# Kernel optimization log

Hardware: AMD Instinct MI355X
Metric: run time of the kernel (lower is better)

Reference implementation:

```python
import jax, jax.numpy as jnp
from jax import lax
import numpy as np

H = 64  # hidden_dim


def _lstm_dir(x, W_ih, W_hh, b, reverse):
    # x: [B,T,I]; W_ih: [4H,I]; W_hh: [4H,H]; b: [4H] (b_ih+b_hh combined)
    B = x.shape[0]
    xp = jnp.einsum('bti,gi->btg', x, W_ih) + b          # [B,T,4H]
    xp = jnp.swapaxes(xp, 0, 1)                          # [T,B,4H]

    def step(carry, xt):
        h, c = carry
        g = xt + h @ W_hh.T                              # [B,4H]
        i, f, gg, o = jnp.split(g, 4, axis=-1)           # PyTorch gate order i,f,g,o
        i = jax.nn.sigmoid(i)
        f = jax.nn.sigmoid(f)
        gg = jnp.tanh(gg)
        o = jax.nn.sigmoid(o)
        c = f * c + i * gg
        h = o * jnp.tanh(c)
        return (h, c), h

    init = (jnp.zeros((B, H), x.dtype), jnp.zeros((B, H), x.dtype))
    _, hs = lax.scan(step, init, xp, reverse=reverse)    # outputs aligned to original positions
    return jnp.swapaxes(hs, 0, 1)                        # [B,T,H]


def _bilstm_layer(x, Wih_f, Whh_f, b_f, Wih_b, Whh_b, b_b):
    fwd = _lstm_dir(x, Wih_f, Whh_f, b_f, reverse=False)
    bwd = _lstm_dir(x, Wih_b, Whh_b, b_b, reverse=True)
    return jnp.concatenate([fwd, bwd], axis=-1)          # [B,T,2H]


def setup_inputs() -> dict:
    key = jax.random.key(0)
    ks = jax.random.split(key, 16)
    s = 0.1
    d = {}
    d['x'] = jax.random.normal(ks[0], (512, 512, 4), dtype=jnp.float32)
    # layer 0 (input size 4), forward / backward directions
    d['Wih_l0_f'] = jax.random.normal(ks[1], (4 * H, 4)) * s
    d['Whh_l0_f'] = jax.random.normal(ks[2], (4 * H, H)) * s
    d['b_l0_f'] = jax.random.normal(ks[3], (4 * H,)) * s
    d['Wih_l0_b'] = jax.random.normal(ks[4], (4 * H, 4)) * s
    d['Whh_l0_b'] = jax.random.normal(ks[5], (4 * H, H)) * s
    d['b_l0_b'] = jax.random.normal(ks[6], (4 * H,)) * s
    # layer 1 (input size 2H = 128)
    d['Wih_l1_f'] = jax.random.normal(ks[7], (4 * H, 2 * H)) * s
    d['Whh_l1_f'] = jax.random.normal(ks[8], (4 * H, H)) * s
    d['b_l1_f'] = jax.random.normal(ks[9], (4 * H,)) * s
    d['Wih_l1_b'] = jax.random.normal(ks[10], (4 * H, 2 * H)) * s
    d['Whh_l1_b'] = jax.random.normal(ks[11], (4 * H, H)) * s
    d['b_l1_b'] = jax.random.normal(ks[12], (4 * H,)) * s
    # final linear: 2H -> 1
    d['fc_w'] = jax.random.normal(ks[13], (1, 2 * H)) * s
    d['fc_b'] = jax.random.normal(ks[14], (1,)) * s
    return d


def reference(x, Wih_l0_f, Whh_l0_f, b_l0_f, Wih_l0_b, Whh_l0_b, b_l0_b,
              Wih_l1_f, Whh_l1_f, b_l1_f, Wih_l1_b, Whh_l1_b, b_l1_b,
              fc_w, fc_b):
    h0 = _bilstm_layer(x, Wih_l0_f, Whh_l0_f, b_l0_f, Wih_l0_b, Whh_l0_b, b_l0_b)
    h1 = _bilstm_layer(h0, Wih_l1_f, Whh_l1_f, b_l1_f, Wih_l1_b, Whh_l1_b, b_l1_b)
    pooled = jnp.mean(h1, axis=1)                        # [B,2H]
    return pooled @ fc_w.T + fc_b                        # [B,1]
```

## Files before the change

kernel.cpp:

```cpp
#include <hip/hip_runtime.h>

#define H  64
#define TT 512
#define BB 512
#define CSTR 80
#define UCH 16
#define XSTRF 260
#define NCHUNK (TT / UCH)

typedef _Float16 half8 __attribute__((ext_vector_type(8)));
typedef float    f32x4 __attribute__((ext_vector_type(4)));

__device__ __forceinline__ float frcp(float x) { return __builtin_amdgcn_rcpf(x); }
__device__ __forceinline__ float sigm(float x) { return frcp(1.f + __expf(-x)); }
__device__ __forceinline__ float tanh_fast(float x) { return 1.f - 2.f * frcp(__expf(2.f * x) + 1.f); }

__device__ __forceinline__ void step_barrier() {
    asm volatile("s_waitcnt lgkmcnt(0)\n\ts_barrier" ::: "memory");
}

__global__ __launch_bounds__(256) void xpad_prep(const float* __restrict__ x,
                                                 _Float16* __restrict__ xpad) {
    int gid = blockIdx.x * 256 + threadIdx.x;
    int row = gid >> 2, q = gid & 3;
    half8 v = {0,0,0,0,0,0,0,0};
    if (q == 0) {
        float4 xv = ((const float4*)x)[row];
        v[0] = (_Float16)xv.x; v[1] = (_Float16)xv.y;
        v[2] = (_Float16)xv.z; v[3] = (_Float16)xv.w;
    }
    *(half8*)(xpad + (size_t)row * 32 + q * 8) = v;
}

__global__ __launch_bounds__(256, 1) void lstm_l0(
    const _Float16* __restrict__ xpad,
    const float* __restrict__ WihF, const float* __restrict__ WhhF, const float* __restrict__ bF,
    const float* __restrict__ WihB, const float* __restrict__ WhhB, const float* __restrict__ bB,
    _Float16* __restrict__ out0)
{
    const int dir = blockIdx.x & 1;
    const int b0  = (blockIdx.x >> 1) * 4;
    const int tid = threadIdx.x;
    const int w = tid >> 6, l = tid & 63, m = l & 15, q = l >> 4;
    const int ch  = m & 3;
    const int ubo = m >> 2;
    const int uo  = w * 16 + ubo * 4 + q;

    const float* Wih = dir ? WihB : WihF;
    const float* Whh = dir ? WhhB : WhhF;
    const float* bia = dir ? bB   : bF;

    half8 Ah[4][2];
#pragma unroll
    for (int ub = 0; ub < 4; ++ub) {
        const int wrow = (m & 3) * 64 + (w * 16 + ub * 4 + (m >> 2));
#pragma unroll
        for (int s2 = 0; s2 < 2; ++s2) {
            const float* src = Whh + wrow * 64 + s2 * 32 + q * 8;
            half8 tmp;
#pragma unroll
            for (int j = 0; j < 8; ++j) tmp[j] = (_Float16)src[j];
            Ah[ub][s2] = tmp;
        }
    }

    half8 Bg[4];
    float bvj[4];
#pragma unroll
    for (int j = 0; j < 4; ++j) {
        const int n  = w * 64 + j * 16 + m;
        const int gr = (n & 3) * 64 + (n >> 2);
        bvj[j] = bia[gr];
        half8 tmp;
#pragma unroll
        for (int jj = 0; jj < 8; ++jj) {
            int k = q * 8 + jj;
            tmp[jj] = (k < 4) ? (_Float16)Wih[gr * 4 + k] : (_Float16)0.f;
        }
        Bg[j] = tmp;
    }

    __shared__ __align__(16) float xp[4][UCH][XSTRF];
    __shared__ __align__(16) _Float16 hbuf[2][4][CSTR];
    for (int i = tid; i < 2 * 4 * CSTR / 2; i += 256) ((unsigned int*)hbuf)[i] = 0u;
    __syncthreads();

    float c = 0.f;
    int p = 0;

    half8 a[4];
    {
        const int tA = dir ? (TT - 1 - m) : m;
#pragma unroll
        for (int cc = 0; cc < 4; ++cc)
            a[cc] = *(const half8*)(xpad + (size_t)((b0 + cc) * TT + tA) * 32 + q * 8);
    }

    for (int chunk = 0; chunk < NCHUNK; ++chunk) {
        const int c0 = chunk * UCH;

#pragma unroll
        for (int cc = 0; cc < 4; ++cc) {
#pragma unroll
            for (int j = 0; j < 4; ++j) {
                f32x4 acc = {bvj[j], bvj[j], bvj[j], bvj[j]};
                acc = __builtin_amdgcn_mfma_f32_16x16x32_f16(a[cc], Bg[j], acc, 0, 0, 0);
#pragma unroll
                for (int i = 0; i < 4; ++i)
                    xp[cc][q * 4 + i][w * 64 + j * 16 + m] = acc[i];
            }
        }
        if (chunk + 1 < NCHUNK) {
            const int c0n = c0 + UCH;
            const int tA = dir ? (TT - 1 - (c0n + m)) : (c0n + m);
#pragma unroll
            for (int cc = 0; cc < 4; ++cc)
                a[cc] = *(const half8*)(xpad + (size_t)((b0 + cc) * TT + tA) * 32 + q * 8);
        }

        f32x4 xv = *(const f32x4*)&xp[ch][0][uo * 4];
        for (int u = 0; u < UCH; ++u) {
            int un = (u + 1 < UCH) ? (u + 1) : u;
            f32x4 xn = *(const f32x4*)&xp[ch][un][uo * 4];

            half8 ah0 = *(const half8*)&hbuf[p][ch][q * 8];
            half8 ah1 = *(const half8*)&hbuf[p][ch][32 + q * 8];

            f32x4 g_own;
#pragma unroll
            for (int ub = 0; ub < 4; ++ub) {
                f32x4 g = __builtin_amdgcn_mfma_f32_16x16x32_f16(Ah[ub][0], ah0, xv, 0, 0, 0);
                g       = __builtin_amdgcn_mfma_f32_16x16x32_f16(Ah[ub][1], ah1, g, 0, 0, 0);
                if (ub == ubo) g_own = g;
            }

            float e_i = sigm(g_own[0]), e_f = sigm(g_own[1]);
            float e_g = tanh_fast(g_own[2]), e_o = sigm(g_own[3]);
            c = e_f * c + e_i * e_g;
            float hh = e_o * tanh_fast(c);

            const int tg = dir ? (TT - 1 - (c0 + u)) : (c0 + u);
            out0[((size_t)(b0 + ch) * TT + tg) * 128 + dir * 64 + uo] = (_Float16)hh;
            hbuf[p ^ 1][ch][uo] = (_Float16)hh;
            step_barrier();
            p ^= 1; xv = xn;
        }
    }
}

__global__ __launch_bounds__(256, 1) void lstm_l1(
    const _Float16* __restrict__ out0,
    const float* __restrict__ WihF, const float* __restrict__ WhhF, const float* __restrict__ bF,
    const float* __restrict__ WihB, const float* __restrict__ WhhB, const float* __restrict__ bB,
    float* __restrict__ pooled)
{
    const int dir = blockIdx.x & 1;
    const int b0  = (blockIdx.x >> 1) * 4;
    const int tid = threadIdx.x;
    const int w = tid >> 6, l = tid & 63, m = l & 15, q = l >> 4;
    const int ch  = m & 3;
    const int ubo = m >> 2;
    const int uo  = w * 16 + ubo * 4 + q;

    const float* Wih = dir ? WihB : WihF;
    const float* Whh = dir ? WhhB : WhhF;
    const float* bia = dir ? bB   : bF;

    half8 Ah[4][2];
#pragma unroll
    for (int ub = 0; ub < 4; ++ub) {
        const int wrow = (m & 3) * 64 + (w * 16 + ub * 4 + (m >> 2));
#pragma unroll
        for (int s2 = 0; s2 < 2; ++s2) {
            const float* src = Whh + wrow * 64 + s2 * 32 + q * 8;
            half8 tmp;
#pragma unroll
            for (int j = 0; j < 8; ++j) tmp[j] = (_Float16)src[j];
            Ah[ub][s2] = tmp;
        }
    }

    half8 Bg[4][4];
    float bvj[4];
#pragma unroll
    for (int j = 0; j < 4; ++j) {
        const int n  = w * 64 + j * 16 + m;
        const int gr = (n & 3) * 64 + (n >> 2);
        bvj[j] = bia[gr];
#pragma unroll
        for (int k4 = 0; k4 < 4; ++k4) {
            const float* src = Wih + gr * 128 + k4 * 32 + q * 8;
            half8 tmp;
#pragma unroll
            for (int jj = 0; jj < 8; ++jj) tmp[jj] = (_Float16)src[jj];
            Bg[j][k4] = tmp;
        }
    }

    __shared__ __align__(16) float xp[4][UCH][XSTRF];
    __shared__ __align__(16) _Float16 hbuf[2][4][CSTR];
    for (int i = tid; i < 2 * 4 * CSTR / 2; i += 256) ((unsigned int*)hbuf)[i] = 0u;
    __syncthreads();

    float c = 0.f, hs = 0.f;
    int p = 0;

    half8 a[4][4];
    {
        const int tA = dir ? (TT - 1 - m) : m;
#pragma unroll
        for (int cc = 0; cc < 4; ++cc) {
            const _Float16* arow = out0 + (size_t)((b0 + cc) * TT + tA) * 128 + q * 8;
#pragma unroll
            for (int k4 = 0; k4 < 4; ++k4)
                a[cc][k4] = *(const half8*)(arow + k4 * 32);
        }
    }

    for (int chunk = 0; chunk < NCHUNK; ++chunk) {
        const int c0 = chunk * UCH;

#pragma unroll
        for (int cc = 0; cc < 4; ++cc) {
#pragma unroll
            for (int j = 0; j < 4; ++j) {
                f32x4 acc = {bvj[j], bvj[j], bvj[j], bvj[j]};
                acc = __builtin_amdgcn_mfma_f32_16x16x32_f16(a[cc][0], Bg[j][0], acc, 0, 0, 0);
                acc = __builtin_amdgcn_mfma_f32_16x16x32_f16(a[cc][1], Bg[j][1], acc, 0, 0, 0);
                acc = __builtin_amdgcn_mfma_f32_16x16x32_f16(a[cc][2], Bg[j][2], acc, 0, 0, 0);
                acc = __builtin_amdgcn_mfma_f32_16x16x32_f16(a[cc][3], Bg[j][3], acc, 0, 0, 0);
#pragma unroll
                for (int i = 0; i < 4; ++i)
                    xp[cc][q * 4 + i][w * 64 + j * 16 + m] = acc[i];
            }
        }
        if (chunk + 1 < NCHUNK) {
            const int c0n = c0 + UCH;
            const int tA = dir ? (TT - 1 - (c0n + m)) : (c0n + m);
#pragma unroll
            for (int cc = 0; cc < 4; ++cc) {
                const _Float16* arow = out0 + (size_t)((b0 + cc) * TT + tA) * 128 + q * 8;
#pragma unroll
                for (int k4 = 0; k4 < 4; ++k4)
                    a[cc][k4] = *(const half8*)(arow + k4 * 32);
            }
        }

        f32x4 xv = *(const f32x4*)&xp[ch][0][uo * 4];
        for (int u = 0; u < UCH; ++u) {
            int un = (u + 1 < UCH) ? (u + 1) : u;
            f32x4 xn = *(const f32x4*)&xp[ch][un][uo * 4];

            half8 ah0 = *(const half8*)&hbuf[p][ch][q * 8];
            half8 ah1 = *(const half8*)&hbuf[p][ch][32 + q * 8];

            f32x4 g_own;
#pragma unroll
            for (int ub = 0; ub < 4; ++ub) {
                f32x4 g = __builtin_amdgcn_mfma_f32_16x16x32_f16(Ah[ub][0], ah0, xv, 0, 0, 0);
                g       = __builtin_amdgcn_mfma_f32_16x16x32_f16(Ah[ub][1], ah1, g, 0, 0, 0);
                if (ub == ubo) g_own = g;
            }

            float e_i = sigm(g_own[0]), e_f = sigm(g_own[1]);
            float e_g = tanh_fast(g_own[2]), e_o = sigm(g_own[3]);
            c = e_f * c + e_i * e_g;
            float hh = e_o * tanh_fast(c);
            hs += hh;

            hbuf[p ^ 1][ch][uo] = (_Float16)hh;
            step_barrier();
            p ^= 1; xv = xn;
        }
    }

    pooled[(size_t)(b0 + ch) * 128 + dir * 64 + uo] = hs;
}

__global__ __launch_bounds__(64) void fc_head(
    const float* __restrict__ pooled,
    const float* __restrict__ fcw, const float* __restrict__ fcb,
    float* __restrict__ out)
{
    const int b = blockIdx.x;
    const int l = threadIdx.x;
    float v = pooled[b * 128 + l] * fcw[l] + pooled[b * 128 + 64 + l] * fcw[64 + l];
#pragma unroll
    for (int o = 32; o > 0; o >>= 1) v += __shfl_down(v, o);
    if (l == 0) out[b] = v * (1.f / (float)TT) + fcb[0];
}

extern "C" void kernel_launch(void* const* d_in, const int* in_sizes, int n_in,
                              void* d_out, int out_size, void* d_ws, size_t ws_size,
                              hipStream_t stream) {
    const float* x       = (const float*)d_in[0];
    const float* Wih_l0f = (const float*)d_in[1];
    const float* Whh_l0f = (const float*)d_in[2];
    const float* b_l0f   = (const float*)d_in[3];
    const float* Wih_l0b = (const float*)d_in[4];
    const float* Whh_l0b = (const float*)d_in[5];
    const float* b_l0b   = (const float*)d_in[6];
    const float* Wih_l1f = (const float*)d_in[7];
    const float* Whh_l1f = (const float*)d_in[8];
    const float* b_l1f   = (const float*)d_in[9];
    const float* Wih_l1b = (const float*)d_in[10];
    const float* Whh_l1b = (const float*)d_in[11];
    const float* b_l1b   = (const float*)d_in[12];
    const float* fcw     = (const float*)d_in[13];
    const float* fcb     = (const float*)d_in[14];

    const size_t o_xpad   = 0;
    const size_t o_out0   = o_xpad + (size_t)BB * TT * 32 * 2;
    const size_t o_pooled = o_out0 + (size_t)BB * TT * 128 * 2;

    _Float16* xpad   = (_Float16*)((char*)d_ws + o_xpad);
    _Float16* out0   = (_Float16*)((char*)d_ws + o_out0);
    float*    pooled = (float*)((char*)d_ws + o_pooled);

    xpad_prep<<<(BB * TT * 4) / 256, 256, 0, stream>>>(x, xpad);
    lstm_l0<<<(BB / 4) * 2, 256, 0, stream>>>(xpad, Wih_l0f, Whh_l0f, b_l0f,
                                              Wih_l0b, Whh_l0b, b_l0b, out0);
    lstm_l1<<<(BB / 4) * 2, 256, 0, stream>>>(out0, Wih_l1f, Whh_l1f, b_l1f,
                                              Wih_l1b, Whh_l1b, b_l1b, pooled);
    fc_head<<<BB, 64, 0, stream>>>(pooled, fcw, fcb, (float*)d_out);
}
```

Measured before the change: 450.8 us.

## Remap gate rows per MFMA tile, fold exp2 scales into weights, vectorize stores

Reorders the recurrent and input weight rows so each of the four MFMA output tiles holds one gate type. Each lane now updates four hidden units directly instead of selecting one tile's result and discarding the rest. The -log2e and 2·log2e factors are folded into the fp16 weights and biases, so the sigmoid and tanh use raw exp2 plus reciprocal, and the cell state is kept in a scaled domain. Hidden-state, output and pooled writes become half4/float4 vector stores from a quarter of the lanes. The trade-off is four times the transcendental work per lane per step on the serial critical path. A barrier is also added after the per-chunk xp writes.

```diff
diff --git a/kernel.cpp b/kernel.cpp
--- a/kernel.cpp
+++ b/kernel.cpp
@@ -5,15 +5,20 @@
 #define BB 512
 #define CSTR 80
 #define UCH 16
-#define XSTRF 260
+#define XROW 260
+#define XCH  (UCH*XROW + 8)
 #define NCHUNK (TT / UCH)
 
 typedef _Float16 half8 __attribute__((ext_vector_type(8)));
+typedef _Float16 half4 __attribute__((ext_vector_type(4)));
 typedef float    f32x4 __attribute__((ext_vector_type(4)));
 
+#define LOG2E 1.4426950408889634f
+#define TWOL  2.8853900817779268f
+#define FOURL 5.7707801635558536f
+
 __device__ __forceinline__ float frcp(float x) { return __builtin_amdgcn_rcpf(x); }
-__device__ __forceinline__ float sigm(float x) { return frcp(1.f + __expf(-x)); }
-__device__ __forceinline__ float tanh_fast(float x) { return 1.f - 2.f * frcp(__expf(2.f * x) + 1.f); }
+__device__ __forceinline__ float ex2(float x)  { return __builtin_amdgcn_exp2f(x); }
 
 __device__ __forceinline__ void step_barrier() {
     asm volatile("s_waitcnt lgkmcnt(0)\n\ts_barrier" ::: "memory");
@@ -42,9 +47,7 @@
     const int b0  = (blockIdx.x >> 1) * 4;
     const int tid = threadIdx.x;
     const int w = tid >> 6, l = tid & 63, m = l & 15, q = l >> 4;
-    const int ch  = m & 3;
-    const int ubo = m >> 2;
-    const int uo  = w * 16 + ubo * 4 + q;
+    const int ch = m & 3;
 
     const float* Wih = dir ? WihB : WihF;
     const float* Whh = dir ? WhhB : WhhF;
@@ -52,40 +55,41 @@
 
     half8 Ah[4][2];
 #pragma unroll
-    for (int ub = 0; ub < 4; ++ub) {
-        const int wrow = (m & 3) * 64 + (w * 16 + ub * 4 + (m >> 2));
+    for (int t = 0; t < 4; ++t) {
+        const float st = (t == 2) ? TWOL : -LOG2E;
+        const int wrow = t * 64 + w * 16 + m;
 #pragma unroll
         for (int s2 = 0; s2 < 2; ++s2) {
             const float* src = Whh + wrow * 64 + s2 * 32 + q * 8;
             half8 tmp;
 #pragma unroll
-            for (int j = 0; j < 8; ++j) tmp[j] = (_Float16)src[j];
-            Ah[ub][s2] = tmp;
-        }
-    }
-
+            for (int j = 0; j < 8; ++j) tmp[j] = (_Float16)(src[j] * st);
+            Ah[t][s2] = tmp;
+        }
+    }
+
+    const float sw = (w == 2) ? TWOL : -LOG2E;
     half8 Bg[4];
     float bvj[4];
 #pragma unroll
     for (int j = 0; j < 4; ++j) {
-        const int n  = w * 64 + j * 16 + m;
-        const int gr = (n & 3) * 64 + (n >> 2);
-        bvj[j] = bia[gr];
+        const int n = w * 64 + j * 16 + m;
+        bvj[j] = bia[n] * sw;
         half8 tmp;
 #pragma unroll
         for (int jj = 0; jj < 8; ++jj) {
             int k = q * 8 + jj;
-            tmp[jj] = (k < 4) ? (_Float16)Wih[gr * 4 + k] : (_Float16)0.f;
+            tmp[jj] = (k < 4) ? (_Float16)(Wih[n * 4 + k] * sw) : (_Float16)0.f;
         }
         Bg[j] = tmp;
     }
 
-    __shared__ __align__(16) float xp[4][UCH][XSTRF];
+    __shared__ __align__(16) float xp[4 * XCH];
     __shared__ __align__(16) _Float16 hbuf[2][4][CSTR];
     for (int i = tid; i < 2 * 4 * CSTR / 2; i += 256) ((unsigned int*)hbuf)[i] = 0u;
     __syncthreads();
 
-    float c = 0.f;
+    float cp[4] = {0.f, 0.f, 0.f, 0.f};
     int p = 0;
 
     half8 a[4];
@@ -107,43 +111,64 @@
                 acc = __builtin_amdgcn_mfma_f32_16x16x32_f16(a[cc], Bg[j], acc, 0, 0, 0);
 #pragma unroll
                 for (int i = 0; i < 4; ++i)
-                    xp[cc][q * 4 + i][w * 64 + j * 16 + m] = acc[i];
+                    xp[cc * XCH + (q * 4 + i) * XROW + w * 64 + j * 16 + m] = acc[i];
             }
         }
         if (chunk + 1 < NCHUNK) {
-            const int c0n = c0 + UCH;
-            const int tA = dir ? (TT - 1 - (c0n + m)) : (c0n + m);
+            const int tA = dir ? (TT - 1 - (c0 + UCH + m)) : (c0 + UCH + m);
 #pragma unroll
             for (int cc = 0; cc < 4; ++cc)
                 a[cc] = *(const half8*)(xpad + (size_t)((b0 + cc) * TT + tA) * 32 + q * 8);
         }
-
-        f32x4 xv = *(const f32x4*)&xp[ch][0][uo * 4];
+        step_barrier();
+
+        f32x4 xv[4];
+#pragma unroll
+        for (int t = 0; t < 4; ++t)
+            xv[t] = *(const f32x4*)&xp[ch * XCH + t * 64 + w * 16 + q * 4];
+
         for (int u = 0; u < UCH; ++u) {
-            int un = (u + 1 < UCH) ? (u + 1) : u;
-            f32x4 xn = *(const f32x4*)&xp[ch][un][uo * 4];
-
             half8 ah0 = *(const half8*)&hbuf[p][ch][q * 8];
             half8 ah1 = *(const half8*)&hbuf[p][ch][32 + q * 8];
 
-            f32x4 g_own;
-#pragma unroll
-            for (int ub = 0; ub < 4; ++ub) {
-                f32x4 g = __builtin_amdgcn_mfma_f32_16x16x32_f16(Ah[ub][0], ah0, xv, 0, 0, 0);
-                g       = __builtin_amdgcn_mfma_f32_16x16x32_f16(Ah[ub][1], ah1, g, 0, 0, 0);
-                if (ub == ubo) g_own = g;
-            }
-
-            float e_i = sigm(g_own[0]), e_f = sigm(g_own[1]);
-            float e_g = tanh_fast(g_own[2]), e_o = sigm(g_own[3]);
-            c = e_f * c + e_i * e_g;
-            float hh = e_o * tanh_fast(c);
-
-            const int tg = dir ? (TT - 1 - (c0 + u)) : (c0 + u);
-            out0[((size_t)(b0 + ch) * TT + tg) * 128 + dir * 64 + uo] = (_Float16)hh;
-            hbuf[p ^ 1][ch][uo] = (_Float16)hh;
+            const int un = (u + 1 < UCH) ? (u + 1) : u;
+            f32x4 xn[4];
+#pragma unroll
+            for (int t = 0; t < 4; ++t)
+                xn[t] = *(const f32x4*)&xp[ch * XCH + un * XROW + t * 64 + w * 16 + q * 4];
+
+            f32x4 g[4];
+#pragma unroll
+            for (int t = 0; t < 4; ++t) {
+                f32x4 acc = __builtin_amdgcn_mfma_f32_16x16x32_f16(Ah[t][0], ah0, xv[t], 0, 0, 0);
+                acc       = __builtin_amdgcn_mfma_f32_16x16x32_f16(Ah[t][1], ah1, acc,  0, 0, 0);
+                g[t] = acc;
+            }
+
+            float hh[4];
+#pragma unroll
+            for (int i = 0; i < 4; ++i) {
+                float e_i = frcp(1.f + ex2(g[0][i]));
+                float e_f = frcp(1.f + ex2(g[1][i]));
+                float tg  = TWOL - FOURL * frcp(1.f + ex2(g[2][i]));
+                float e_o = frcp(1.f + ex2(g[3][i]));
+                cp[i] = e_f * cp[i] + e_i * tg;
+                float r = frcp(1.f + ex2(cp[i]));
+                hh[i] = e_o * fmaf(-2.f, r, 1.f);
+            }
+
+            if (m < 4) {
+                half4 hv;
+                hv[0] = (_Float16)hh[0]; hv[1] = (_Float16)hh[1];
+                hv[2] = (_Float16)hh[2]; hv[3] = (_Float16)hh[3];
+                const int tg_t = dir ? (TT - 1 - (c0 + u)) : (c0 + u);
+                *(half4*)&out0[((size_t)(b0 + m) * TT + tg_t) * 128 + dir * 64 + w * 16 + q * 4] = hv;
+                *(half4*)&hbuf[p ^ 1][m][w * 16 + q * 4] = hv;
+            }
             step_barrier();
-            p ^= 1; xv = xn;
+            p ^= 1;
+#pragma unroll
+            for (int t = 0; t < 4; ++t) xv[t] = xn[t];
         }
     }
 }
@@ -158,9 +183,7 @@
     const int b0  = (blockIdx.x >> 1) * 4;
     const int tid = threadIdx.x;
     const int w = tid >> 6, l = tid & 63, m = l & 15, q = l >> 4;
-    const int ch  = m & 3;
-    const int ubo = m >> 2;
-    const int uo  = w * 16 + ubo * 4 + q;
+    const int ch = m & 3;
 
     const float* Wih = dir ? WihB : WihF;
     const float* Whh = dir ? WhhB : WhhF;
@@ -168,41 +191,43 @@
 
     half8 Ah[4][2];
 #pragma unroll
-    for (int ub = 0; ub < 4; ++ub) {
-        const int wrow = (m & 3) * 64 + (w * 16 + ub * 4 + (m >> 2));
+    for (int t = 0; t < 4; ++t) {
+        const float st = (t == 2) ? TWOL : -LOG2E;
+        const int wrow = t * 64 + w * 16 + m;
 #pragma unroll
         for (int s2 = 0; s2 < 2; ++s2) {
             const float* src = Whh + wrow * 64 + s2 * 32 + q * 8;
             half8 tmp;
 #pragma unroll
-            for (int j = 0; j < 8; ++j) tmp[j] = (_Float16)src[j];
-            Ah[ub][s2] = tmp;
-        }
-    }
-
+            for (int j = 0; j < 8; ++j) tmp[j] = (_Float16)(src[j] * st);
+            Ah[t][s2] = tmp;
+        }
+    }
+
+    const float sw = (w == 2) ? TWOL : -LOG2E;
     half8 Bg[4][4];
     float bvj[4];
 #pragma unroll
     for (int j = 0; j < 4; ++j) {
-        const int n  = w * 64 + j * 16 + m;
-        const int gr = (n & 3) * 64 + (n >> 2);
-        bvj[j] = bia[gr];
+        const int n = w * 64 + j * 16 + m;
+        bvj[j] = bia[n] * sw;
 #pragma unroll
         for (int k4 = 0; k4 < 4; ++k4) {
-            const float* src = Wih + gr * 128 + k4 * 32 + q * 8;
+            const float* src = Wih + n * 128 + k4 * 32 + q * 8;
             half8 tmp;
 #pragma unroll
-            for (int jj = 0; jj < 8; ++jj) tmp[jj] = (_Float16)src[jj];
+            for (int jj = 0; jj < 8; ++jj) tmp[jj] = (_Float16)(src[jj] * sw);
             Bg[j][k4] = tmp;
         }
     }
 
-    __shared__ __align__(16) float xp[4][UCH][XSTRF];
+    __shared__ __align__(16) float xp[4 * XCH];
     __shared__ __align__(16) _Float16 hbuf[2][4][CSTR];
     for (int i = tid; i < 2 * 4 * CSTR / 2; i += 256) ((unsigned int*)hbuf)[i] = 0u;
     __syncthreads();
 
-    float c = 0.f, hs = 0.f;
+    float cp[4] = {0.f, 0.f, 0.f, 0.f};
+    float hs[4] = {0.f, 0.f, 0.f, 0.f};
     int p = 0;
 
     half8 a[4][4];
@@ -231,12 +256,11 @@
                 acc = __builtin_amdgcn_mfma_f32_16x16x32_f16(a[cc][3], Bg[j][3], acc, 0, 0, 0);
 #pragma unroll
                 for (int i = 0; i < 4; ++i)
-                    xp[cc][q * 4 + i][w * 64 + j * 16 + m] = acc[i];
+                    xp[cc * XCH + (q * 4 + i) * XROW + w * 64 + j * 16 + m] = acc[i];
             }
         }
         if (chunk + 1 < NCHUNK) {
-            const int c0n = c0 + UCH;
-            const int tA = dir ? (TT - 1 - (c0n + m)) : (c0n + m);
+            const int tA = dir ? (TT - 1 - (c0 + UCH + m)) : (c0 + UCH + m);
 #pragma unroll
             for (int cc = 0; cc < 4; ++cc) {
                 const _Float16* arow = out0 + (size_t)((b0 + cc) * TT + tA) * 128 + q * 8;
@@ -245,36 +269,61 @@
                     a[cc][k4] = *(const half8*)(arow + k4 * 32);
             }
         }
-
-        f32x4 xv = *(const f32x4*)&xp[ch][0][uo * 4];
+        step_barrier();
+
+        f32x4 xv[4];
+#pragma unroll
+        for (int t = 0; t < 4; ++t)
+            xv[t] = *(const f32x4*)&xp[ch * XCH + t * 64 + w * 16 + q * 4];
+
         for (int u = 0; u < UCH; ++u) {
-            int un = (u + 1 < UCH) ? (u + 1) : u;
-            f32x4 xn = *(const f32x4*)&xp[ch][un][uo * 4];
-
             half8 ah0 = *(const half8*)&hbuf[p][ch][q * 8];
             half8 ah1 = *(const half8*)&hbuf[p][ch][32 + q * 8];
 
-            f32x4 g_own;
-#pragma unroll
-            for (int ub = 0; ub < 4; ++ub) {
-                f32x4 g = __builtin_amdgcn_mfma_f32_16x16x32_f16(Ah[ub][0], ah0, xv, 0, 0, 0);
-                g       = __builtin_amdgcn_mfma_f32_16x16x32_f16(Ah[ub][1], ah1, g, 0, 0, 0);
-                if (ub == ubo) g_own = g;
-            }
-
-            float e_i = sigm(g_own[0]), e_f = sigm(g_own[1]);
-            float e_g = tanh_fast(g_own[2]), e_o = sigm(g_own[3]);
-            c = e_f * c + e_i * e_g;
-            float hh = e_o * tanh_fast(c);
-            hs += hh;
-
-            hbuf[p ^ 1][ch][uo] = (_Float16)hh;
+            const int un = (u + 1 < UCH) ? (u + 1) : u;
+            f32x4 xn[4];
+#pragma unroll
+            for (int t = 0; t < 4; ++t)
+                xn[t] = *(const f32x4*)&xp[ch * XCH + un * XROW + t * 64 + w * 16 + q * 4];
+
+            f32x4 g[4];
+#pragma unroll
+            for (int t = 0; t < 4; ++t) {
+                f32x4 acc = __builtin_amdgcn_mfma_f32_16x16x32_f16(Ah[t][0], ah0, xv[t], 0, 0, 0);
+                acc       = __builtin_amdgcn_mfma_f32_16x16x32_f16(Ah[t][1], ah1, acc,  0, 0, 0);
+                g[t] = acc;
+            }
+
+            float hh[4];
+#pragma unroll
+            for (int i = 0; i < 4; ++i) {
+                float e_i = frcp(1.f + ex2(g[0][i]));
+                float e_f = frcp(1.f + ex2(g[1][i]));
+                float tg  = TWOL - FOURL * frcp(1.f + ex2(g[2][i]));
+                float e_o = frcp(1.f + ex2(g[3][i]));
+                cp[i] = e_f * cp[i] + e_i * tg;
+                float r = frcp(1.f + ex2(cp[i]));
+                hh[i] = e_o * fmaf(-2.f, r, 1.f);
+                hs[i] += hh[i];
+            }
+
+            if (m < 4) {
+                half4 hv;
+                hv[0] = (_Float16)hh[0]; hv[1] = (_Float16)hh[1];
+                hv[2] = (_Float16)hh[2]; hv[3] = (_Float16)hh[3];
+                *(half4*)&hbuf[p ^ 1][m][w * 16 + q * 4] = hv;
+            }
             step_barrier();
-            p ^= 1; xv = xn;
-        }
-    }
-
-    pooled[(size_t)(b0 + ch) * 128 + dir * 64 + uo] = hs;
+            p ^= 1;
+#pragma unroll
+            for (int t = 0; t < 4; ++t) xv[t] = xn[t];
+        }
+    }
+
+    if (m < 4) {
+        f32x4 hv = {hs[0], hs[1], hs[2], hs[3]};
+        *(f32x4*)&pooled[(size_t)(b0 + m) * 128 + dir * 64 + w * 16 + q * 4] = hv;
+    }
 }
 
 __global__ __launch_bounds__(64) void fc_head(
```

New measurement: 549.1 us. 1.22x slower.

## Interleave next-chunk input projection into recurrent steps with double-buffered LDS

Applied to the files above, without the earlier changes.

The input-projection MFMAs for the next chunk are now spread across the 16 recurrent steps of the current chunk and written to a second LDS buffer, with global loads prefetched two chunks ahead. This hides the projection phase that previously sat on the serial path between chunks. Gate scaling by -log2e and 2·log2e is folded into the weights and biases so activations use exp2 directly. The gate-to-lane mapping is changed to use a select instead of an accumulator-initialized MFMA. This costs more registers and LDS, and removes the explicit sync between chunks, relying on the per-step barrier instead.

```diff
diff --git a/kernel.cpp b/kernel.cpp
--- a/kernel.cpp
+++ b/kernel.cpp
@@ -5,18 +5,30 @@
 #define BB 512
 #define CSTR 80
 #define UCH 16
-#define XSTRF 260
+#define XROW 264
+#define XCH  (UCH * XROW + 8)
 #define NCHUNK (TT / UCH)
 
 typedef _Float16 half8 __attribute__((ext_vector_type(8)));
 typedef float    f32x4 __attribute__((ext_vector_type(4)));
 
+#define LOG2E 1.4426950408889634f
+#define TWOL  2.8853900817779268f
+#define FOURL 5.7707801635558536f
+
+#define MFMA16 __builtin_amdgcn_mfma_f32_16x16x32_f16
+
 __device__ __forceinline__ float frcp(float x) { return __builtin_amdgcn_rcpf(x); }
-__device__ __forceinline__ float sigm(float x) { return frcp(1.f + __expf(-x)); }
-__device__ __forceinline__ float tanh_fast(float x) { return 1.f - 2.f * frcp(__expf(2.f * x) + 1.f); }
+__device__ __forceinline__ float ex2(float x)  { return __builtin_amdgcn_exp2f(x); }
 
 __device__ __forceinline__ void step_barrier() {
     asm volatile("s_waitcnt lgkmcnt(0)\n\ts_barrier" ::: "memory");
+}
+
+__device__ __forceinline__ float sel4(f32x4 v, bool lo, bool hi) {
+    float a = lo ? v[1] : v[0];
+    float b = lo ? v[3] : v[2];
+    return hi ? b : a;
 }
 
 __global__ __launch_bounds__(256) void xpad_prep(const float* __restrict__ x,
@@ -31,6 +43,56 @@
     }
     *(half8*)(xpad + (size_t)row * 32 + q * 8) = v;
 }
+
+
+#define L0_CHUNK(CIDX, XPR, XPW, AUSE, ALOAD)                                   \
+    {                                                                           \
+        const int c_ = (CIDX);                                                  \
+        if (c_ + 2 < NCHUNK) {                                                  \
+            const int tL = dir ? (TT - 1 - ((c_ + 2) * UCH + m))                \
+                               : ((c_ + 2) * UCH + m);                          \
+            _Pragma("unroll")                                                   \
+            for (int cc = 0; cc < 4; ++cc)                                      \
+                ALOAD[cc] = *(const half8*)(xpad +                              \
+                    (size_t)((b0 + cc) * TT + tL) * 32 + q * 8);                \
+        }                                                                       \
+        _Pragma("unroll")                                                       \
+        for (int u = 0; u < UCH; ++u) {                                         \
+            half8 ah0 = *(const half8*)&hbuf[p][ch][q * 8];                     \
+            half8 ah1 = *(const half8*)&hbuf[p][ch][32 + q * 8];                \
+            f32x4 xq = *(const f32x4*)&XPR[ch * XCH + u * XROW + uo * 4];       \
+            f32x4 g0 = MFMA16(Ah[0][0], ah0, vz, 0, 0, 0);                      \
+            g0       = MFMA16(Ah[0][1], ah1, g0, 0, 0, 0);                      \
+            f32x4 g1 = MFMA16(Ah[1][0], ah0, vz, 0, 0, 0);                      \
+            g1       = MFMA16(Ah[1][1], ah1, g1, 0, 0, 0);                      \
+            f32x4 g2 = MFMA16(Ah[2][0], ah0, vz, 0, 0, 0);                      \
+            g2       = MFMA16(Ah[2][1], ah1, g2, 0, 0, 0);                      \
+            f32x4 g3 = MFMA16(Ah[3][0], ah0, vz, 0, 0, 0);                      \
+            g3       = MFMA16(Ah[3][1], ah1, g3, 0, 0, 0);                      \
+            {                                \
+                f32x4 acc = bb[u & 3];                                          \
+                acc = MFMA16(Wg[u & 3], AUSE[u >> 2], acc, 0, 0, 0);            \
+                *(f32x4*)&XPW[(u >> 2) * XCH + m * XROW +                       \
+                              (w * 16 + (u & 3) * 4 + q) * 4] = acc;            \
+            }                                                                   \
+            float gi = sel4(g0, sLo, sHi) + xq[0];                              \
+            float gf = sel4(g1, sLo, sHi) + xq[1];                              \
+            float gg = sel4(g2, sLo, sHi) + xq[2];                              \
+            float go = sel4(g3, sLo, sHi) + xq[3];                              \
+            float e_i = frcp(1.f + ex2(gi));                                    \
+            float e_f = frcp(1.f + ex2(gf));                                    \
+            float tg  = TWOL - FOURL * frcp(1.f + ex2(gg));                     \
+            float e_o = frcp(1.f + ex2(go));                                    \
+            cp = e_f * cp + e_i * tg;                                           \
+            float hh = e_o * fmaf(-2.f, frcp(1.f + ex2(cp)), 1.f);              \
+            const int tg_t = dir ? (TT - 1 - (c_ * UCH + u)) : (c_ * UCH + u);  \
+            out0[((size_t)(b0 + ch) * TT + tg_t) * 128 + dir * 64 + uo] =       \
+                (_Float16)hh;                                                   \
+            hbuf[p ^ 1][ch][uo] = (_Float16)hh;                                 \
+            step_barrier();                                                     \
+            p ^= 1;                                                             \
+        }                                                                       \
+    }
 
 __global__ __launch_bounds__(256, 1) void lstm_l0(
     const _Float16* __restrict__ xpad,
@@ -42,9 +104,10 @@
     const int b0  = (blockIdx.x >> 1) * 4;
     const int tid = threadIdx.x;
     const int w = tid >> 6, l = tid & 63, m = l & 15, q = l >> 4;
-    const int ch  = m & 3;
-    const int ubo = m >> 2;
-    const int uo  = w * 16 + ubo * 4 + q;
+    const int ch = m & 3;
+    const int i0 = m >> 2;
+    const int uo = w * 16 + q * 4 + i0;
+    const bool sLo = (i0 & 1) != 0, sHi = (i0 & 2) != 0;
 
     const float* Wih = dir ? WihB : WihF;
     const float* Whh = dir ? WhhB : WhhF;
@@ -52,101 +115,131 @@
 
     half8 Ah[4][2];
 #pragma unroll
-    for (int ub = 0; ub < 4; ++ub) {
-        const int wrow = (m & 3) * 64 + (w * 16 + ub * 4 + (m >> 2));
+    for (int t = 0; t < 4; ++t) {
+        const float st = (t == 2) ? TWOL : -LOG2E;
+        const int wrow = t * 64 + w * 16 + m;
 #pragma unroll
         for (int s2 = 0; s2 < 2; ++s2) {
             const float* src = Whh + wrow * 64 + s2 * 32 + q * 8;
             half8 tmp;
 #pragma unroll
-            for (int j = 0; j < 8; ++j) tmp[j] = (_Float16)src[j];
-            Ah[ub][s2] = tmp;
-        }
-    }
-
-    half8 Bg[4];
-    float bvj[4];
+            for (int j = 0; j < 8; ++j) tmp[j] = (_Float16)(src[j] * st);
+            Ah[t][s2] = tmp;
+        }
+    }
+
+    const float sm = ((m & 3) == 2) ? TWOL : -LOG2E;
+    half8 Wg[4];
 #pragma unroll
     for (int j = 0; j < 4; ++j) {
-        const int n  = w * 64 + j * 16 + m;
-        const int gr = (n & 3) * 64 + (n >> 2);
-        bvj[j] = bia[gr];
+        const int gr = (m & 3) * 64 + w * 16 + j * 4 + (m >> 2);
         half8 tmp;
 #pragma unroll
         for (int jj = 0; jj < 8; ++jj) {
             int k = q * 8 + jj;
-            tmp[jj] = (k < 4) ? (_Float16)Wih[gr * 4 + k] : (_Float16)0.f;
-        }
-        Bg[j] = tmp;
-    }
-
-    __shared__ __align__(16) float xp[4][UCH][XSTRF];
+            tmp[jj] = (k < 4) ? (_Float16)(Wih[gr * 4 + k] * sm) : (_Float16)0.f;
+        }
+        Wg[j] = tmp;
+    }
+
+    f32x4 bb[4];
+#pragma unroll
+    for (int j = 0; j < 4; ++j) {
+        const int ub = w * 16 + j * 4 + q;
+        bb[j][0] = bia[ub]       * -LOG2E;
+        bb[j][1] = bia[64 + ub]  * -LOG2E;
+        bb[j][2] = bia[128 + ub] * TWOL;
+        bb[j][3] = bia[192 + ub] * -LOG2E;
+    }
+
+    const f32x4 vz = {0.f, 0.f, 0.f, 0.f};
+
+    __shared__ __align__(16) float xpA[4 * XCH];
+    __shared__ __align__(16) float xpB[4 * XCH];
     __shared__ __align__(16) _Float16 hbuf[2][4][CSTR];
     for (int i = tid; i < 2 * 4 * CSTR / 2; i += 256) ((unsigned int*)hbuf)[i] = 0u;
-    __syncthreads();
-
-    float c = 0.f;
+
+    float cp = 0.f;
     int p = 0;
 
-    half8 a[4];
+    half8 aR[2][4];
     {
-        const int tA = dir ? (TT - 1 - m) : m;
-#pragma unroll
-        for (int cc = 0; cc < 4; ++cc)
-            a[cc] = *(const half8*)(xpad + (size_t)((b0 + cc) * TT + tA) * 32 + q * 8);
-    }
-
-    for (int chunk = 0; chunk < NCHUNK; ++chunk) {
-        const int c0 = chunk * UCH;
-
+        const int t0 = dir ? (TT - 1 - m) : m;
+        const int t1 = dir ? (TT - 1 - (UCH + m)) : (UCH + m);
 #pragma unroll
         for (int cc = 0; cc < 4; ++cc) {
-#pragma unroll
-            for (int j = 0; j < 4; ++j) {
-                f32x4 acc = {bvj[j], bvj[j], bvj[j], bvj[j]};
-                acc = __builtin_amdgcn_mfma_f32_16x16x32_f16(a[cc], Bg[j], acc, 0, 0, 0);
-#pragma unroll
-                for (int i = 0; i < 4; ++i)
-                    xp[cc][q * 4 + i][w * 64 + j * 16 + m] = acc[i];
-            }
-        }
-        if (chunk + 1 < NCHUNK) {
-            const int c0n = c0 + UCH;
-            const int tA = dir ? (TT - 1 - (c0n + m)) : (c0n + m);
-#pragma unroll
-            for (int cc = 0; cc < 4; ++cc)
-                a[cc] = *(const half8*)(xpad + (size_t)((b0 + cc) * TT + tA) * 32 + q * 8);
-        }
-
-        f32x4 xv = *(const f32x4*)&xp[ch][0][uo * 4];
-        for (int u = 0; u < UCH; ++u) {
-            int un = (u + 1 < UCH) ? (u + 1) : u;
-            f32x4 xn = *(const f32x4*)&xp[ch][un][uo * 4];
-
-            half8 ah0 = *(const half8*)&hbuf[p][ch][q * 8];
-            half8 ah1 = *(const half8*)&hbuf[p][ch][32 + q * 8];
-
-            f32x4 g_own;
-#pragma unroll
-            for (int ub = 0; ub < 4; ++ub) {
-                f32x4 g = __builtin_amdgcn_mfma_f32_16x16x32_f16(Ah[ub][0], ah0, xv, 0, 0, 0);
-                g       = __builtin_amdgcn_mfma_f32_16x16x32_f16(Ah[ub][1], ah1, g, 0, 0, 0);
-                if (ub == ubo) g_own = g;
-            }
-
-            float e_i = sigm(g_own[0]), e_f = sigm(g_own[1]);
-            float e_g = tanh_fast(g_own[2]), e_o = sigm(g_own[3]);
-            c = e_f * c + e_i * e_g;
-            float hh = e_o * tanh_fast(c);
-
-            const int tg = dir ? (TT - 1 - (c0 + u)) : (c0 + u);
-            out0[((size_t)(b0 + ch) * TT + tg) * 128 + dir * 64 + uo] = (_Float16)hh;
-            hbuf[p ^ 1][ch][uo] = (_Float16)hh;
-            step_barrier();
-            p ^= 1; xv = xn;
-        }
-    }
-}
+            aR[0][cc] = *(const half8*)(xpad + (size_t)((b0 + cc) * TT + t0) * 32 + q * 8);
+            aR[1][cc] = *(const half8*)(xpad + (size_t)((b0 + cc) * TT + t1) * 32 + q * 8);
+        }
+#pragma unroll
+        for (int pp = 0; pp < 16; ++pp) {
+            const int cc = pp >> 2, j = pp & 3;
+            f32x4 acc = bb[j];
+            acc = MFMA16(Wg[j], aR[0][cc], acc, 0, 0, 0);
+            *(f32x4*)&xpA[cc * XCH + m * XROW + (w * 16 + j * 4 + q) * 4] = acc;
+        }
+        __syncthreads();
+    }
+
+    for (int c = 0; c < NCHUNK; c += 2) {
+        L0_CHUNK(c,     xpA, xpB, aR[1], aR[0]);
+        L0_CHUNK(c + 1, xpB, xpA, aR[0], aR[1]);
+    }
+}
+
+#define L1_CHUNK(CIDX, XPR, XPW, AUSE, ALOAD)                                   \
+    {                                                                           \
+        const int c_ = (CIDX);                                                  \
+        if (c_ + 2 < NCHUNK) {                                                  \
+            const int tL = dir ? (TT - 1 - ((c_ + 2) * UCH + m))                \
+                               : ((c_ + 2) * UCH + m);                          \
+            _Pragma("unroll")                                                   \
+            for (int cc = 0; cc < 4; ++cc) {                                    \
+                const _Float16* arow = out0 +                                   \
+                    (size_t)((b0 + cc) * TT + tL) * 128 + q * 8;                \
+                _Pragma("unroll")                                               \
+                for (int k4 = 0; k4 < 4; ++k4)                                  \
+                    ALOAD[cc][k4] = *(const half8*)(arow + k4 * 32);            \
+            }                                                                   \
+        }                                                                       \
+        _Pragma("unroll")                                                       \
+        for (int u = 0; u < UCH; ++u) {                                         \
+            half8 ah0 = *(const half8*)&hbuf[p][ch][q * 8];                     \
+            half8 ah1 = *(const half8*)&hbuf[p][ch][32 + q * 8];                \
+            f32x4 xq = *(const f32x4*)&XPR[ch * XCH + u * XROW + uo * 4];       \
+            f32x4 g0 = MFMA16(Ah[0][0], ah0, vz, 0, 0, 0);                      \
+            g0       = MFMA16(Ah[0][1], ah1, g0, 0, 0, 0);                      \
+            f32x4 g1 = MFMA16(Ah[1][0], ah0, vz, 0, 0, 0);                      \
+            g1       = MFMA16(Ah[1][1], ah1, g1, 0, 0, 0);                      \
+            f32x4 g2 = MFMA16(Ah[2][0], ah0, vz, 0, 0, 0);                      \
+            g2       = MFMA16(Ah[2][1], ah1, g2, 0, 0, 0);                      \
+            f32x4 g3 = MFMA16(Ah[3][0], ah0, vz, 0, 0, 0);                      \
+            g3       = MFMA16(Ah[3][1], ah1, g3, 0, 0, 0);                      \
+            {                                   \
+                f32x4 acc = bb[u & 3];                                          \
+                acc = MFMA16(Wg[u & 3][0], AUSE[u >> 2][0], acc, 0, 0, 0);      \
+                acc = MFMA16(Wg[u & 3][1], AUSE[u >> 2][1], acc, 0, 0, 0);      \
+                acc = MFMA16(Wg[u & 3][2], AUSE[u >> 2][2], acc, 0, 0, 0);      \
+                acc = MFMA16(Wg[u & 3][3], AUSE[u >> 2][3], acc, 0, 0, 0);      \
+                *(f32x4*)&XPW[(u >> 2) * XCH + m * XROW +                       \
+                              (w * 16 + (u & 3) * 4 + q) * 4] = acc;            \
+            }                                                                   \
+            float gi = sel4(g0, sLo, sHi) + xq[0];                              \
+            float gf = sel4(g1, sLo, sHi) + xq[1];                              \
+            float gg = sel4(g2, sLo, sHi) + xq[2];                              \
+            float go = sel4(g3, sLo, sHi) + xq[3];                              \
+            float e_i = frcp(1.f + ex2(gi));                                    \
+            float e_f = frcp(1.f + ex2(gf));                                    \
+            float tg  = TWOL - FOURL * frcp(1.f + ex2(gg));                     \
+            float e_o = frcp(1.f + ex2(go));                                    \
+            cp = e_f * cp + e_i * tg;                                           \
+            float hh = e_o * fmaf(-2.f, frcp(1.f + ex2(cp)), 1.f);              \
+            hs += hh;                                                           \
+            hbuf[p ^ 1][ch][uo] = (_Float16)hh;                                 \
+            step_barrier();                                                     \
+            p ^= 1;                                                             \
+        }                                                                       \
+    }
 
 __global__ __launch_bounds__(256, 1) void lstm_l1(
     const _Float16* __restrict__ out0,
@@ -158,9 +251,10 @@
     const int b0  = (blockIdx.x >> 1) * 4;
     const int tid = threadIdx.x;
     const int w = tid >> 6, l = tid & 63, m = l & 15, q = l >> 4;
-    const int ch  = m & 3;
-    const int ubo = m >> 2;
-    const int uo  = w * 16 + ubo * 4 + q;
+    const int ch = m & 3;
+    const int i0 = m >> 2;
+    const int uo = w * 16 + q * 4 + i0;
+    const bool sLo = (i0 & 1) != 0, sHi = (i0 & 2) != 0;
 
     const float* Wih = dir ? WihB : WihF;
     const float* Whh = dir ? WhhB : WhhF;
@@ -168,110 +262,84 @@
 
     half8 Ah[4][2];
 #pragma unroll
-    for (int ub = 0; ub < 4; ++ub) {
-        const int wrow = (m & 3) * 64 + (w * 16 + ub * 4 + (m >> 2));
+    for (int t = 0; t < 4; ++t) {
+        const float st = (t == 2) ? TWOL : -LOG2E;
+        const int wrow = t * 64 + w * 16 + m;
 #pragma unroll
         for (int s2 = 0; s2 < 2; ++s2) {
             const float* src = Whh + wrow * 64 + s2 * 32 + q * 8;
             half8 tmp;
 #pragma unroll
-            for (int j = 0; j < 8; ++j) tmp[j] = (_Float16)src[j];
-            Ah[ub][s2] = tmp;
-        }
-    }
-
-    half8 Bg[4][4];
-    float bvj[4];
+            for (int j = 0; j < 8; ++j) tmp[j] = (_Float16)(src[j] * st);
+            Ah[t][s2] = tmp;
+        }
+    }
+
+    const float sm = ((m & 3) == 2) ? TWOL : -LOG2E;
+    half8 Wg[4][4];
 #pragma unroll
     for (int j = 0; j < 4; ++j) {
-        const int n  = w * 64 + j * 16 + m;
-        const int gr = (n & 3) * 64 + (n >> 2);
-        bvj[j] = bia[gr];
+        const int gr = (m & 3) * 64 + w * 16 + j * 4 + (m >> 2);
 #pragma unroll
         for (int k4 = 0; k4 < 4; ++k4) {
             const float* src = Wih + gr * 128 + k4 * 32 + q * 8;
             half8 tmp;
 #pragma unroll
-            for (int jj = 0; jj < 8; ++jj) tmp[jj] = (_Float16)src[jj];
-            Bg[j][k4] = tmp;
-        }
-    }
-
-    __shared__ __align__(16) float xp[4][UCH][XSTRF];
+            for (int jj = 0; jj < 8; ++jj) tmp[jj] = (_Float16)(src[jj] * sm);
+            Wg[j][k4] = tmp;
+        }
+    }
+
+    f32x4 bb[4];
+#pragma unroll
+    for (int j = 0; j < 4; ++j) {
+        const int ub = w * 16 + j * 4 + q;
+        bb[j][0] = bia[ub]       * -LOG2E;
+        bb[j][1] = bia[64 + ub]  * -LOG2E;
+        bb[j][2] = bia[128 + ub] * TWOL;
+        bb[j][3] = bia[192 + ub] * -LOG2E;
+    }
+
+    const f32x4 vz = {0.f, 0.f, 0.f, 0.f};
+
+    __shared__ __align__(16) float xpA[4 * XCH];
+    __shared__ __align__(16) float xpB[4 * XCH];
     __shared__ __align__(16) _Float16 hbuf[2][4][CSTR];
     for (int i = tid; i < 2 * 4 * CSTR / 2; i += 256) ((unsigned int*)hbuf)[i] = 0u;
-    __syncthreads();
-
-    float c = 0.f, hs = 0.f;
+
+    float cp = 0.f, hs = 0.f;
     int p = 0;
 
-    half8 a[4][4];
+    half8 aR[2][4][4];
     {
-        const int tA = dir ? (TT - 1 - m) : m;
+        const int t0 = dir ? (TT - 1 - m) : m;
+        const int t1 = dir ? (TT - 1 - (UCH + m)) : (UCH + m);
 #pragma unroll
         for (int cc = 0; cc < 4; ++cc) {
-            const _Float16* arow = out0 + (size_t)((b0 + cc) * TT + tA) * 128 + q * 8;
-#pragma unroll
-            for (int k4 = 0; k4 < 4; ++k4)
-                a[cc][k4] = *(const half8*)(arow + k4 * 32);
-        }
-    }
-
-    for (int chunk = 0; chunk < NCHUNK; ++chunk) {
-        const int c0 = chunk * UCH;
-
-#pragma unroll
-        for (int cc = 0; cc < 4; ++cc) {
-#pragma unroll
-            for (int j = 0; j < 4; ++j) {
-                f32x4 acc = {bvj[j], bvj[j], bvj[j], bvj[j]};
-                acc = __builtin_amdgcn_mfma_f32_16x16x32_f16(a[cc][0], Bg[j][0], acc, 0, 0, 0);
-                acc = __builtin_amdgcn_mfma_f32_16x16x32_f16(a[cc][1], Bg[j][1], acc, 0, 0, 0);
-                acc = __builtin_amdgcn_mfma_f32_16x16x32_f16(a[cc][2], Bg[j][2], acc, 0, 0, 0);
-                acc = __builtin_amdgcn_mfma_f32_16x16x32_f16(a[cc][3], Bg[j][3], acc, 0, 0, 0);
-#pragma unroll
-                for (int i = 0; i < 4; ++i)
-                    xp[cc][q * 4 + i][w * 64 + j * 16 + m] = acc[i];
+            const _Float16* r0 = out0 + (size_t)((b0 + cc) * TT + t0) * 128 + q * 8;
+            const _Float16* r1 = out0 + (size_t)((b0 + cc) * TT + t1) * 128 + q * 8;
+#pragma unroll
+            for (int k4 = 0; k4 < 4; ++k4) {
+                aR[0][cc][k4] = *(const half8*)(r0 + k4 * 32);
+                aR[1][cc][k4] = *(const half8*)(r1 + k4 * 32);
             }
         }
-        if (chunk + 1 < NCHUNK) {
-            const int c0n = c0 + UCH;
-            const int tA = dir ? (TT - 1 - (c0n + m)) : (c0n + m);
-#pragma unroll
-            for (int cc = 0; cc < 4; ++cc) {
-                const _Float16* arow = out0 + (size_t)((b0 + cc) * TT + tA) * 128 + q * 8;
-#pragma unroll
-                for (int k4 = 0; k4 < 4; ++k4)
-                    a[cc][k4] = *(const half8*)(arow + k4 * 32);
-            }
-        }
-
-        f32x4 xv = *(const f32x4*)&xp[ch][0][uo * 4];
-        for (int u = 0; u < UCH; ++u) {
-            int un = (u + 1 < UCH) ? (u + 1) : u;
-            f32x4 xn = *(const f32x4*)&xp[ch][un][uo * 4];
-
-            half8 ah0 = *(const half8*)&hbuf[p][ch][q * 8];
-            half8 ah1 = *(const half8*)&hbuf[p][ch][32 + q * 8];
-
-            f32x4 g_own;
-#pragma unroll
-            for (int ub = 0; ub < 4; ++ub) {
-                f32x4 g = __builtin_amdgcn_mfma_f32_16x16x32_f16(Ah[ub][0], ah0, xv, 0, 0, 0);
-                g       = __builtin_amdgcn_mfma_f32_16x16x32_f16(Ah[ub][1], ah1, g, 0, 0, 0);
-                if (ub == ubo) g_own = g;
-            }
-
-            float e_i = sigm(g_own[0]), e_f = sigm(g_own[1]);
-            float e_g = tanh_fast(g_own[2]), e_o = sigm(g_own[3]);
-            c = e_f * c + e_i * e_g;
-            float hh = e_o * tanh_fast(c);
-            hs += hh;
-
-            hbuf[p ^ 1][ch][uo] = (_Float16)hh;
-            step_barrier();
-            p ^= 1; xv = xn;
-        }
+#pragma unroll
+        for (int pp = 0; pp < 16; ++pp) {
+            const int cc = pp >> 2, j = pp & 3;
+            f32x4 acc = bb[j];
+            acc = MFMA16(Wg[j][0], aR[0][cc][0], acc, 0, 0, 0);
+            acc = MFMA16(Wg[j][1], aR[0][cc][1], acc, 0, 0, 0);
+            acc = MFMA16(Wg[j][2], aR[0][cc][2], acc, 0, 0, 0);
+            acc = MFMA16(Wg[j][3], aR[0][cc][3], acc, 0, 0, 0);
+            *(f32x4*)&xpA[cc * XCH + m * XROW + (w * 16 + j * 4 + q) * 4] = acc;
+        }
+        __syncthreads();
+    }
+
+    for (int c = 0; c < NCHUNK; c += 2) {
+        L1_CHUNK(c,     xpA, xpB, aR[1], aR[0]);
+        L1_CHUNK(c + 1, xpB, xpA, aR[0], aR[1]);
     }
 
     pooled[(size_t)(b0 + ch) * 128 + dir * 64 + uo] = hs;
```

New measurement: 401.8 us. 1.12x faster.
